# Kernel optimization log

Hardware: AMD Instinct MI355X
Metric: run time of the kernel (lower is better)

Reference implementation:

```python
import jax, jax.numpy as jnp
import numpy as np
import itertools


def _comb_indices(F, k):
    # Flattened combination indices: for each of C(F,k) combinations, its k
    # member feature ids, concatenated. Row i of the original one-hot crmatrix
    # has a single 1 at column idx[i], so x @ crmatrix^T == gather by idx.
    return np.fromiter(itertools.chain(*itertools.combinations(range(F), k)),
                       dtype=np.int32)


def setup_inputs() -> dict:
    key = jax.random.key(0)
    x = jax.random.normal(key, (32, 4096, 32), dtype=jnp.float32)  # [B, T, F]
    return {"x": x, "k": 2}


def reference(x, k):
    F = x.shape[2]
    idx = jnp.asarray(_comb_indices(F, k))          # [ncr] = [k * C(F,k)]
    # Faithful to K.dot(x, crmatrix) with one-hot crmatrix: a feature gather.
    return jnp.take(x, idx, axis=2)                 # [B, T, ncr]
```

## Files before the change

kernel.cpp:

```cpp
#include <hip/hip_runtime.h>


#define FDIM 32
#define NCR 992
#define G_PER_ROW 248
#define ROWS_PER_BLOCK 8
#define BLOCK 256

typedef float f32x4 __attribute__((ext_vector_type(4)));

__global__ __launch_bounds__(BLOCK)
void comb_gather_kernel(const float* __restrict__ x,
                        float* __restrict__ out,
                        int nrows) {
    __shared__ float lds[ROWS_PER_BLOCK * FDIM];

    const int tid  = threadIdx.x;
    const int row0 = blockIdx.x * ROWS_PER_BLOCK;
    const bool full = (row0 + ROWS_PER_BLOCK) <= nrows;

    if (tid < (ROWS_PER_BLOCK * FDIM) / 4) {
        const f32x4* src = reinterpret_cast<const f32x4*>(x + (size_t)row0 * FDIM);
        if (full) {
            reinterpret_cast<f32x4*>(lds)[tid] = src[tid];
        } else {
            int row_of_load = row0 + (tid * 4) / FDIM;
            if (row_of_load < nrows)
                reinterpret_cast<f32x4*>(lds)[tid] = src[tid];
        }
    }

    int feat[4];
    const int g = tid;
    if (g < G_PER_ROW) {
        #pragma unroll
        for (int u = 0; u < 4; ++u) {
            int j   = g * 4 + u;
            int c   = j >> 1;
            int pos = j & 1;
            int i = 0, cum = 0;
            while (cum + (FDIM - 1 - i) <= c) { cum += FDIM - 1 - i; ++i; }
            int second = c - cum + i + 1;
            feat[u] = pos ? second : i;
        }
    }
    __syncthreads();

    if (g >= G_PER_ROW) return;

    if (full) {
        f32x4* outp = reinterpret_cast<f32x4*>(out + (size_t)row0 * NCR) + g;
        #pragma unroll
        for (int r = 0; r < ROWS_PER_BLOCK; ++r) {
            const float* rowp = lds + r * FDIM;
            f32x4 v;
            v.x = rowp[feat[0]];
            v.y = rowp[feat[1]];
            v.z = rowp[feat[2]];
            v.w = rowp[feat[3]];
            __builtin_nontemporal_store(v, outp);
            outp += NCR / 4;
        }
    } else {
        #pragma unroll
        for (int r = 0; r < ROWS_PER_BLOCK; ++r) {
            int row = row0 + r;
            if (row >= nrows) break;
            const float* rowp = lds + r * FDIM;
            f32x4 v;
            v.x = rowp[feat[0]];
            v.y = rowp[feat[1]];
            v.z = rowp[feat[2]];
            v.w = rowp[feat[3]];
            __builtin_nontemporal_store(
                v, reinterpret_cast<f32x4*>(out + (size_t)row * NCR) + g);
        }
    }
}

extern "C" void kernel_launch(void* const* d_in, const int* in_sizes, int n_in,
                              void* d_out, int out_size, void* d_ws, size_t ws_size,
                              hipStream_t stream) {
    const float* x  = (const float*)d_in[0];
    float* out      = (float*)d_out;
    int nrows = in_sizes[0] / FDIM;
    int grid  = (nrows + ROWS_PER_BLOCK - 1) / ROWS_PER_BLOCK;
    hipLaunchKernelGGL(comb_gather_kernel, dim3(grid), dim3(BLOCK), 0, stream,
                       x, out, nrows);
}
```

Before: 104.4 us.

## Double rows per block and compute combination indices in closed form

Each block now handles 16 rows instead of 8, and all 256 threads stage the input with 2-float loads. The per-thread while-loop that decodes combination indices is replaced by a sqrt-based closed-form inverse with a one-step correction, applied once per pair of combinations. This halves the block count and amortizes index setup over more rows, at the cost of narrower loads and a float-rounding correction that must hold at every index.

```diff
diff --git a/kernel.cpp b/kernel.cpp
--- a/kernel.cpp
+++ b/kernel.cpp
@@ -4,10 +4,11 @@
 #define FDIM 32
 #define NCR 992
 #define G_PER_ROW 248
-#define ROWS_PER_BLOCK 8
+#define ROWS_PER_BLOCK 16
 #define BLOCK 256
 
 typedef float f32x4 __attribute__((ext_vector_type(4)));
+typedef float f32x2 __attribute__((ext_vector_type(2)));
 
 __global__ __launch_bounds__(BLOCK)
 void comb_gather_kernel(const float* __restrict__ x,
@@ -19,30 +20,35 @@
     const int row0 = blockIdx.x * ROWS_PER_BLOCK;
     const bool full = (row0 + ROWS_PER_BLOCK) <= nrows;
 
-    if (tid < (ROWS_PER_BLOCK * FDIM) / 4) {
-        const f32x4* src = reinterpret_cast<const f32x4*>(x + (size_t)row0 * FDIM);
+    {
+        const f32x2* src = reinterpret_cast<const f32x2*>(x + (size_t)row0 * FDIM);
         if (full) {
-            reinterpret_cast<f32x4*>(lds)[tid] = src[tid];
+            reinterpret_cast<f32x2*>(lds)[tid] = src[tid];
         } else {
-            int row_of_load = row0 + (tid * 4) / FDIM;
+            int row_of_load = row0 + (tid * 2) / FDIM;
             if (row_of_load < nrows)
-                reinterpret_cast<f32x4*>(lds)[tid] = src[tid];
+                reinterpret_cast<f32x2*>(lds)[tid] = src[tid];
         }
     }
 
     int feat[4];
     const int g = tid;
     if (g < G_PER_ROW) {
-        #pragma unroll
-        for (int u = 0; u < 4; ++u) {
-            int j   = g * 4 + u;
-            int c   = j >> 1;
-            int pos = j & 1;
-            int i = 0, cum = 0;
-            while (cum + (FDIM - 1 - i) <= c) { cum += FDIM - 1 - i; ++i; }
-            int second = c - cum + i + 1;
-            feat[u] = pos ? second : i;
-        }
+        const int c0 = 2 * g;
+        float s = sqrtf(3969.0f - 8.0f * (float)c0);
+        int i0 = (int)((63.0f - s) * 0.5f);
+        if (i0 < 0) i0 = 0;
+        int st0  = (i0 * (63 - i0)) >> 1;
+        int stn0 = ((i0 + 1) * (62 - i0)) >> 1;
+        if (stn0 <= c0) { i0++; st0 = stn0; stn0 = ((i0 + 1) * (62 - i0)) >> 1; }
+        else if (st0 > c0) { i0--; stn0 = st0; st0 = (i0 * (63 - i0)) >> 1; }
+        feat[0] = i0;
+        feat[1] = c0 - st0 + i0 + 1;
+        const int c1 = c0 + 1;
+        int i1 = i0, st1 = st0;
+        if (stn0 <= c1) { i1 = i0 + 1; st1 = stn0; }
+        feat[2] = i1;
+        feat[3] = c1 - st1 + i1 + 1;
     }
     __syncthreads();
 
```

After: 101.1 us (median of 2 runs). -3.1%, faster.
